# Performance work log

Hardware: AMD Instinct MI355X
Metric: run time of the kernel (lower is better)

The kernel has to match this reference:

```python
import jax, jax.numpy as jnp
import numpy as np

NUM_STEPS = 5
N_NODES = 50000
N_EDGES = 1250000
D_FEAT = 64


def setup_inputs() -> dict:
    key = jax.random.key(0)
    k1, k2, k3, k4 = jax.random.split(key, 4)
    x = jax.random.normal(k1, (N_NODES, D_FEAT), dtype=jnp.float32)
    edge_vals = jax.random.uniform(k2, (N_EDGES,), dtype=jnp.float32)
    edge_rows = jax.random.randint(k3, (N_EDGES,), 0, N_NODES, dtype=jnp.int32)
    edge_cols = jax.random.randint(k4, (N_EDGES,), 0, N_NODES, dtype=jnp.int32)
    return {"x": x, "edge_vals": edge_vals, "edge_rows": edge_rows, "edge_cols": edge_cols}


def reference(x, edge_vals, edge_rows, edge_cols):
    # Repeated SpMM: x <- A @ x, with A given in COO form (rows, cols, vals).
    # torch.sparse.mm(A, x)[i] = sum_{e: rows[e]==i} vals[e] * x[cols[e]]
    n = x.shape[0]

    def spmm(h):
        msgs = edge_vals[:, None] * h[edge_cols]          # [E, D] gather + scale
        return jax.ops.segment_sum(msgs, edge_rows, num_segments=n)  # [N, D] scatter-add

    for _ in range(NUM_STEPS):
        x = spmm(x)
    return x
```

## Files before the change

kernel.cpp:

```cpp
#include <hip/hip_runtime.h>
#include <hip/hip_fp16.h>
#include <stdint.h>

#define D_FEAT 64
#define CH 4096
#define BKT_BITS 8

__global__ __launch_bounds__(256) void bhist_kernel(const int* __restrict__ rows,
                                                    int* __restrict__ block_hist,
                                                    int n_edges, int nb) {
    __shared__ int cnt[256];
    cnt[threadIdx.x] = 0;
    __syncthreads();
    int beg = blockIdx.x * CH;
    int end = min(beg + CH, n_edges);
    for (int i = beg + threadIdx.x; i < end; i += 256)
        atomicAdd(&cnt[rows[i] >> BKT_BITS], 1);
    __syncthreads();
    if (threadIdx.x < nb)
        block_hist[blockIdx.x * nb + threadIdx.x] = cnt[threadIdx.x];
}

__global__ __launch_bounds__(256) void bscan1_kernel(int* __restrict__ block_hist,
                                                     int* __restrict__ btot,
                                                     int nchunks, int nb) {
    __shared__ int buf[256];
    int j = blockIdx.x;
    int t = threadIdx.x;
    int c0 = 2 * t, c1 = 2 * t + 1;
    int v0 = (c0 < nchunks) ? block_hist[(size_t)c0 * nb + j] : 0;
    int v1 = (c1 < nchunks) ? block_hist[(size_t)c1 * nb + j] : 0;
    int loc = v0 + v1;
    buf[t] = loc;
    __syncthreads();
    for (int off = 1; off < 256; off <<= 1) {
        int add = (t >= off) ? buf[t - off] : 0;
        __syncthreads();
        buf[t] += add;
        __syncthreads();
    }
    int excl = buf[t] - loc;
    if (c0 < nchunks) block_hist[(size_t)c0 * nb + j] = excl;
    if (c1 < nchunks) block_hist[(size_t)c1 * nb + j] = excl + v0;
    if (t == 255) btot[j] = buf[255];
}

__global__ __launch_bounds__(256) void bscan2_kernel(const int* __restrict__ btot,
                                                     int* __restrict__ bbase, int nb) {
    __shared__ int buf[256];
    int t = threadIdx.x;
    int v = (t < nb) ? btot[t] : 0;
    buf[t] = v;
    __syncthreads();
    for (int off = 1; off < 256; off <<= 1) {
        int add = (t >= off) ? buf[t - off] : 0;
        __syncthreads();
        buf[t] += add;
        __syncthreads();
    }
    if (t < nb) {
        bbase[t] = buf[t] - v;
        if (t == nb - 1) bbase[nb] = buf[t];
    }
}

__global__ __launch_bounds__(256) void bplace_kernel(const float* __restrict__ vals,
                                                     const int* __restrict__ rows,
                                                     const int* __restrict__ cols,
                                                     const int* __restrict__ block_hist,
                                                     const int* __restrict__ bbase,
                                                     uint2* __restrict__ mid,
                                                     int n_edges, int nb) {
    __shared__ int cnt[256];
    __shared__ int base[256];
    int t = threadIdx.x;
    cnt[t] = 0;
    if (t < nb) base[t] = bbase[t] + block_hist[(size_t)blockIdx.x * nb + t];
    __syncthreads();
    int beg = blockIdx.x * CH;
    int end = min(beg + CH, n_edges);
    for (int i = beg + t; i < end; i += 256) {
        int r = rows[i];
        int b = r >> BKT_BITS;
        int lrank = atomicAdd(&cnt[b], 1);
        __half hv = __float2half_rn(vals[i]);
        unsigned short vb = *reinterpret_cast<unsigned short*>(&hv);
        uint32_t packed = (uint32_t)(cols[i] & 0xFFFF) | ((uint32_t)vb << 16);
        mid[base[b] + lrank] = make_uint2(packed, (uint32_t)r);
    }
}

__global__ __launch_bounds__(256) void bsort_kernel(const uint2* __restrict__ mid,
                                                    const int* __restrict__ bbase,
                                                    uint32_t* __restrict__ edges,
                                                    int* __restrict__ offs,
                                                    int n_nodes, int nb) {
    __shared__ int cnt[256];
    __shared__ int start[256];
    __shared__ int buf[256];
    int j = blockIdx.x;
    int t = threadIdx.x;
    int lo = bbase[j];
    int hi = bbase[j + 1];
    cnt[t] = 0;
    __syncthreads();
    const uint32_t RMASK = (1u << BKT_BITS) - 1u;
    for (int i = lo + t; i < hi; i += 256)
        atomicAdd(&cnt[mid[i].y & RMASK], 1);
    __syncthreads();
    int v = cnt[t];
    buf[t] = v;
    __syncthreads();
    for (int off = 1; off < 256; off <<= 1) {
        int add = (t >= off) ? buf[t - off] : 0;
        __syncthreads();
        buf[t] += add;
        __syncthreads();
    }
    int st = buf[t] - v;
    start[t] = st;
    int rg = (j << BKT_BITS) + t;
    if (rg <= n_nodes) offs[rg] = lo + st;
    __syncthreads();
    cnt[t] = 0;
    __syncthreads();
    for (int i = lo + t; i < hi; i += 256) {
        uint2 e = mid[i];
        int r = (int)(e.y & RMASK);
        int rank = atomicAdd(&cnt[r], 1);
        edges[lo + start[r] + rank] = e.x;
    }
}


__device__ __forceinline__ float unpack_val(uint32_t u) {
    __half_raw hr;
    hr.x = (unsigned short)(u >> 16);
    return __half2float(__half(hr));
}

__device__ __forceinline__ float2 ld_bypass_f2(const float2* p) {
    unsigned long long v = __hip_atomic_load((const unsigned long long*)p,
                                             __ATOMIC_RELAXED, __HIP_MEMORY_SCOPE_AGENT);
    union { unsigned long long u; float2 f; } c;
    c.u = v;
    return c.f;
}
__device__ __forceinline__ __half2 ld_bypass_h2(const __half2* p) {
    uint32_t v = __hip_atomic_load((const uint32_t*)p,
                                   __ATOMIC_RELAXED, __HIP_MEMORY_SCOPE_AGENT);
    union { uint32_t u; __half2 h; } c;
    c.u = v;
    return c.h;
}

template <int K, bool IN_F32>
__device__ __forceinline__ void gfma2(const void* __restrict__ hv,
                                      const uint32_t* __restrict__ edges,
                                      int j, int gl, float2& acc) {
    uint32_t u[K];
#pragma unroll
    for (int k = 0; k < K; ++k) u[k] = edges[j + k];
    float2 hh[K];
#pragma unroll
    for (int k = 0; k < K; ++k) {
        size_t c = (size_t)(u[k] & 0xFFFF);
        if (IN_F32) hh[k] = ld_bypass_f2(((const float2*)hv) + c * 32 + gl);
        else        hh[k] = __half22float2(ld_bypass_h2(((const __half2*)hv) + c * 32 + gl));
    }
#pragma unroll
    for (int k = 0; k < K; ++k) {
        float v = unpack_val(u[k]);
        acc.x = fmaf(v, hh[k].x, acc.x);
        acc.y = fmaf(v, hh[k].y, acc.y);
    }
}

template <bool IN_F32, bool OUT_F32>
__global__ __launch_bounds__(256) void spmm2_kernel(const void* __restrict__ hv,
                                                    const uint32_t* __restrict__ edges,
                                                    const int* __restrict__ offs,
                                                    void* __restrict__ outv, int n_nodes) {
    int wave = (int)(((long long)blockIdx.x * blockDim.x + threadIdx.x) >> 6);
    int lane = threadIdx.x & 63;
    int g = lane >> 5;
    int gl = lane & 31;
    int row = wave * 2 + g;
    if (row >= n_nodes) return;
    int beg = offs[row];
    int end = offs[row + 1];
    float2 acc = make_float2(0.f, 0.f);
    int j = beg;
    for (; j + 8 <= end; j += 8) gfma2<8, IN_F32>(hv, edges, j, gl, acc);
    if (j + 4 <= end) { gfma2<4, IN_F32>(hv, edges, j, gl, acc); j += 4; }
    for (; j < end; ++j) {
        uint32_t u = edges[j];
        size_t c = (size_t)(u & 0xFFFF);
        float2 hh = IN_F32 ? ld_bypass_f2(((const float2*)hv) + c * 32 + gl)
                           : __half22float2(ld_bypass_h2(((const __half2*)hv) + c * 32 + gl));
        float v = unpack_val(u);
        acc.x = fmaf(v, hh.x, acc.x);
        acc.y = fmaf(v, hh.y, acc.y);
    }
    if (OUT_F32) {
        ((float2*)outv)[(size_t)row * 32 + gl] = acc;
    } else {
        ((__half2*)outv)[(size_t)row * 32 + gl] = __float22half2_rn(acc);
    }
}


__global__ void spmm_atomic_kernel(const float* __restrict__ h,
                                   const float* __restrict__ vals,
                                   const int* __restrict__ rows,
                                   const int* __restrict__ cols,
                                   float* __restrict__ out,
                                   int n_edges) {
    long long tid = (long long)blockIdx.x * blockDim.x + threadIdx.x;
    int e = (int)(tid >> 6);
    int d = (int)(tid & 63);
    if (e >= n_edges) return;
    float m = vals[e] * h[(size_t)cols[e] * D_FEAT + d];
    atomicAdd(&out[(size_t)rows[e] * D_FEAT + d], m);
}

extern "C" void kernel_launch(void* const* d_in, const int* in_sizes, int n_in,
                              void* d_out, int out_size, void* d_ws, size_t ws_size,
                              hipStream_t stream) {
    const float* x    = (const float*)d_in[0];
    const float* vals = (const float*)d_in[1];
    const int*   rows = (const int*)d_in[2];
    const int*   cols = (const int*)d_in[3];

    int n_nodes = in_sizes[0] / D_FEAT;
    int n_edges = in_sizes[1];

    float* out = (float*)d_out;

    size_t buf_bytes_f32 = (size_t)n_nodes * D_FEAT * sizeof(float);
    size_t buf_bytes_f16 = (size_t)n_nodes * D_FEAT * sizeof(__half);

    auto align_up = [](size_t v) { return (v + 255) & ~(size_t)255; };

    int nb = (n_nodes + 255) >> BKT_BITS;
    int nchunks = (n_edges + CH - 1) / CH;

    size_t pa_b   = align_up(buf_bytes_f16);
    size_t pb_b   = align_up(buf_bytes_f16);
    size_t mid_b  = align_up((size_t)n_edges * sizeof(uint2));
    size_t region1 = pa_b + pb_b;
    if (mid_b > region1) region1 = mid_b;
    size_t edges_b = align_up((size_t)n_edges * sizeof(uint32_t));
    size_t offs_b  = align_up((size_t)(n_nodes + 1) * sizeof(int));
    size_t bh_b    = align_up((size_t)nchunks * nb * sizeof(int));
    size_t bb_b    = align_up((size_t)(nb + 1) * sizeof(int));
    size_t bt_b    = align_up(256 * sizeof(int));
    size_t need = region1 + edges_b + offs_b + bh_b + bb_b + bt_b;

    if (ws_size < need || n_nodes > 65536 || nchunks > 512) {
        float* ws = (float*)d_ws;
        float* dsts[5] = {out, ws, out, ws, out};
        long long total_threads = (long long)n_edges * D_FEAT;
        int block = 256;
        int grid = (int)((total_threads + block - 1) / block);
        const float* src = x;
        for (int s = 0; s < 5; ++s) {
            hipMemsetAsync(dsts[s], 0, buf_bytes_f32, stream);
            spmm_atomic_kernel<<<grid, block, 0, stream>>>(src, vals, rows, cols,
                                                           dsts[s], n_edges);
            src = dsts[s];
        }
        return;
    }

    char* p = (char*)d_ws;
    char* r1 = p;                        p += region1;
    uint32_t* edges      = (uint32_t*)p; p += edges_b;
    int*      offs       = (int*)p;      p += offs_b;
    int*      block_hist = (int*)p;      p += bh_b;
    int*      bbase      = (int*)p;      p += bb_b;
    int*      btot       = (int*)p;      p += bt_b;

    __half2* pA = (__half2*)r1;
    __half2* pB = (__half2*)(r1 + pa_b);
    uint2*   mid = (uint2*)r1;

    bhist_kernel<<<nchunks, 256, 0, stream>>>(rows, block_hist, n_edges, nb);
    bscan1_kernel<<<nb, 256, 0, stream>>>(block_hist, btot, nchunks, nb);
    bscan2_kernel<<<1, 256, 0, stream>>>(btot, bbase, nb);
    bplace_kernel<<<nchunks, 256, 0, stream>>>(vals, rows, cols, block_hist, bbase,
                                               mid, n_edges, nb);
    bsort_kernel<<<nb, 256, 0, stream>>>(mid, bbase, edges, offs, n_nodes, nb);

    {
        int rows_per_block = 8;
        int grid = (n_nodes + rows_per_block - 1) / rows_per_block;
        spmm2_kernel<true,  false><<<grid, 256, 0, stream>>>(x,  edges, offs, pA, n_nodes);
        spmm2_kernel<false, false><<<grid, 256, 0, stream>>>(pA, edges, offs, pB, n_nodes);
        spmm2_kernel<false, false><<<grid, 256, 0, stream>>>(pB, edges, offs, pA, n_nodes);
        spmm2_kernel<false, false><<<grid, 256, 0, stream>>>(pA, edges, offs, pB, n_nodes);
        spmm2_kernel<false, true ><<<grid, 256, 0, stream>>>(pB, edges, offs, out, n_nodes);
    }
}
```

Measured before the change: 245.8 us.

## Assign one wave per row with 8-edge parallel gathers and shuffle reduction

Rewrites the SpMM kernel so each 64-lane wave handles one row. Eight subgroups of 8 lanes each gather a different edge's feature row with 16-byte vector loads, then the partial sums are combined by xor-shuffles. Ordinary cached loads replace the atomic bypass loads. The change aims for wider memory transactions and more gathers in flight per wave, at the cost of shuffle-reduction overhead and redundant lanes at the store.

```diff
diff --git a/kernel.cpp b/kernel.cpp
--- a/kernel.cpp
+++ b/kernel.cpp
@@ -139,73 +139,102 @@
     return __half2float(__half(hr));
 }
 
-__device__ __forceinline__ float2 ld_bypass_f2(const float2* p) {
-    unsigned long long v = __hip_atomic_load((const unsigned long long*)p,
-                                             __ATOMIC_RELAXED, __HIP_MEMORY_SCOPE_AGENT);
-    union { unsigned long long u; float2 f; } c;
-    c.u = v;
-    return c.f;
-}
-__device__ __forceinline__ __half2 ld_bypass_h2(const __half2* p) {
-    uint32_t v = __hip_atomic_load((const uint32_t*)p,
-                                   __ATOMIC_RELAXED, __HIP_MEMORY_SCOPE_AGENT);
-    union { uint32_t u; __half2 h; } c;
-    c.u = v;
-    return c.h;
-}
-
-template <int K, bool IN_F32>
-__device__ __forceinline__ void gfma2(const void* __restrict__ hv,
-                                      const uint32_t* __restrict__ edges,
-                                      int j, int gl, float2& acc) {
-    uint32_t u[K];
-#pragma unroll
-    for (int k = 0; k < K; ++k) u[k] = edges[j + k];
-    float2 hh[K];
-#pragma unroll
-    for (int k = 0; k < K; ++k) {
-        size_t c = (size_t)(u[k] & 0xFFFF);
-        if (IN_F32) hh[k] = ld_bypass_f2(((const float2*)hv) + c * 32 + gl);
-        else        hh[k] = __half22float2(ld_bypass_h2(((const __half2*)hv) + c * 32 + gl));
-    }
-#pragma unroll
-    for (int k = 0; k < K; ++k) {
-        float v = unpack_val(u[k]);
-        acc.x = fmaf(v, hh[k].x, acc.x);
-        acc.y = fmaf(v, hh[k].y, acc.y);
-    }
+__device__ __forceinline__ float2 h2f(uint32_t w) {
+    __half2 h = *reinterpret_cast<__half2*>(&w);
+    return __half22float2(h);
+}
+
+__device__ __forceinline__ uint32_t f2h2(float a, float b) {
+    __half2 h = __float22half2_rn(make_float2(a, b));
+    return *reinterpret_cast<uint32_t*>(&h);
+}
+
+__device__ __forceinline__ void fma8_h(const uint4& q, float v, float* acc) {
+    float2 f;
+    f = h2f(q.x); acc[0] = fmaf(v, f.x, acc[0]); acc[1] = fmaf(v, f.y, acc[1]);
+    f = h2f(q.y); acc[2] = fmaf(v, f.x, acc[2]); acc[3] = fmaf(v, f.y, acc[3]);
+    f = h2f(q.z); acc[4] = fmaf(v, f.x, acc[4]); acc[5] = fmaf(v, f.y, acc[5]);
+    f = h2f(q.w); acc[6] = fmaf(v, f.x, acc[6]); acc[7] = fmaf(v, f.y, acc[7]);
+}
+
+__device__ __forceinline__ void fma8_f(const float4& q0, const float4& q1, float v, float* acc) {
+    acc[0] = fmaf(v, q0.x, acc[0]); acc[1] = fmaf(v, q0.y, acc[1]);
+    acc[2] = fmaf(v, q0.z, acc[2]); acc[3] = fmaf(v, q0.w, acc[3]);
+    acc[4] = fmaf(v, q1.x, acc[4]); acc[5] = fmaf(v, q1.y, acc[5]);
+    acc[6] = fmaf(v, q1.z, acc[6]); acc[7] = fmaf(v, q1.w, acc[7]);
 }
 
 template <bool IN_F32, bool OUT_F32>
-__global__ __launch_bounds__(256) void spmm2_kernel(const void* __restrict__ hv,
+__global__ __launch_bounds__(256) void spmm8_kernel(const void* __restrict__ hv,
                                                     const uint32_t* __restrict__ edges,
                                                     const int* __restrict__ offs,
                                                     void* __restrict__ outv, int n_nodes) {
-    int wave = (int)(((long long)blockIdx.x * blockDim.x + threadIdx.x) >> 6);
+    int row = (int)(((long long)blockIdx.x * blockDim.x + threadIdx.x) >> 6);
+    if (row >= n_nodes) return;
     int lane = threadIdx.x & 63;
-    int g = lane >> 5;
-    int gl = lane & 31;
-    int row = wave * 2 + g;
-    if (row >= n_nodes) return;
-    int beg = offs[row];
-    int end = offs[row + 1];
-    float2 acc = make_float2(0.f, 0.f);
-    int j = beg;
-    for (; j + 8 <= end; j += 8) gfma2<8, IN_F32>(hv, edges, j, gl, acc);
-    if (j + 4 <= end) { gfma2<4, IN_F32>(hv, edges, j, gl, acc); j += 4; }
-    for (; j < end; ++j) {
-        uint32_t u = edges[j];
-        size_t c = (size_t)(u & 0xFFFF);
-        float2 hh = IN_F32 ? ld_bypass_f2(((const float2*)hv) + c * 32 + gl)
-                           : __half22float2(ld_bypass_h2(((const __half2*)hv) + c * 32 + gl));
-        float v = unpack_val(u);
-        acc.x = fmaf(v, hh.x, acc.x);
-        acc.y = fmaf(v, hh.y, acc.y);
-    }
+    int sg = lane >> 3;
+    int fl = lane & 7;
+
+    int beg = offs[row], end = offs[row + 1];
+    float acc[8] = {0.f, 0.f, 0.f, 0.f, 0.f, 0.f, 0.f, 0.f};
+
+    int j0 = beg;
+    for (; j0 + 16 <= end; j0 += 16) {
+        uint32_t ua = edges[j0 + sg];
+        uint32_t ub = edges[j0 + 8 + sg];
+        if (IN_F32) {
+            const float4* hp = (const float4*)hv;
+            size_t ca = (size_t)(ua & 0xFFFF) * 16 + fl * 2;
+            size_t cb = (size_t)(ub & 0xFFFF) * 16 + fl * 2;
+            float4 qa0 = hp[ca], qa1 = hp[ca + 1];
+            float4 qb0 = hp[cb], qb1 = hp[cb + 1];
+            fma8_f(qa0, qa1, unpack_val(ua), acc);
+            fma8_f(qb0, qb1, unpack_val(ub), acc);
+        } else {
+            const uint4* hp = (const uint4*)hv;
+            uint4 qa = hp[(size_t)(ua & 0xFFFF) * 8 + fl];
+            uint4 qb = hp[(size_t)(ub & 0xFFFF) * 8 + fl];
+            fma8_h(qa, unpack_val(ua), acc);
+            fma8_h(qb, unpack_val(ub), acc);
+        }
+    }
+    for (; j0 < end; j0 += 8) {
+        int j = j0 + sg;
+        if (j < end) {
+            uint32_t u = edges[j];
+            float v = unpack_val(u);
+            if (IN_F32) {
+                const float4* hp = (const float4*)hv;
+                size_t c = (size_t)(u & 0xFFFF) * 16 + fl * 2;
+                float4 q0 = hp[c], q1 = hp[c + 1];
+                fma8_f(q0, q1, v, acc);
+            } else {
+                const uint4* hp = (const uint4*)hv;
+                uint4 q = hp[(size_t)(u & 0xFFFF) * 8 + fl];
+                fma8_h(q, v, acc);
+            }
+        }
+    }
+
+#pragma unroll
+    for (int m = 8; m <= 32; m <<= 1) {
+#pragma unroll
+        for (int i = 0; i < 8; ++i) acc[i] += __shfl_xor(acc[i], m, 64);
+    }
+
     if (OUT_F32) {
-        ((float2*)outv)[(size_t)row * 32 + gl] = acc;
+        float4* op = (float4*)outv + (size_t)row * 16 + fl * 2;
+        if (sg == 0) op[0] = make_float4(acc[0], acc[1], acc[2], acc[3]);
+        else if (sg == 1) op[1] = make_float4(acc[4], acc[5], acc[6], acc[7]);
     } else {
-        ((__half2*)outv)[(size_t)row * 32 + gl] = __float22half2_rn(acc);
+        if (sg == 0) {
+            uint4 o;
+            o.x = f2h2(acc[0], acc[1]);
+            o.y = f2h2(acc[2], acc[3]);
+            o.z = f2h2(acc[4], acc[5]);
+            o.w = f2h2(acc[6], acc[7]);
+            ((uint4*)outv)[(size_t)row * 8 + fl] = o;
+        }
     }
 }
 
@@ -281,9 +310,9 @@
     int*      bbase      = (int*)p;      p += bb_b;
     int*      btot       = (int*)p;      p += bt_b;
 
-    __half2* pA = (__half2*)r1;
-    __half2* pB = (__half2*)(r1 + pa_b);
-    uint2*   mid = (uint2*)r1;
+    __half* pA = (__half*)r1;
+    __half* pB = (__half*)(r1 + pa_b);
+    uint2*  mid = (uint2*)r1;
 
     bhist_kernel<<<nchunks, 256, 0, stream>>>(rows, block_hist, n_edges, nb);
     bscan1_kernel<<<nb, 256, 0, stream>>>(block_hist, btot, nchunks, nb);
@@ -293,12 +322,12 @@
     bsort_kernel<<<nb, 256, 0, stream>>>(mid, bbase, edges, offs, n_nodes, nb);
 
     {
-        int rows_per_block = 8;
+        int rows_per_block = 4;
         int grid = (n_nodes + rows_per_block - 1) / rows_per_block;
-        spmm2_kernel<true,  false><<<grid, 256, 0, stream>>>(x,  edges, offs, pA, n_nodes);
-        spmm2_kernel<false, false><<<grid, 256, 0, stream>>>(pA, edges, offs, pB, n_nodes);
-        spmm2_kernel<false, false><<<grid, 256, 0, stream>>>(pB, edges, offs, pA, n_nodes);
-        spmm2_kernel<false, false><<<grid, 256, 0, stream>>>(pA, edges, offs, pB, n_nodes);
-        spmm2_kernel<false, true ><<<grid, 256, 0, stream>>>(pB, edges, offs, out, n_nodes);
-    }
-}
+        spmm8_kernel<true,  false><<<grid, 256, 0, stream>>>(x,  edges, offs, pA, n_nodes);
+        spmm8_kernel<false, false><<<grid, 256, 0, stream>>>(pA, edges, offs, pB, n_nodes);
+        spmm8_kernel<false, false><<<grid, 256, 0, stream>>>(pB, edges, offs, pA, n_nodes);
+        spmm8_kernel<false, false><<<grid, 256, 0, stream>>>(pA, edges, offs, pB, n_nodes);
+        spmm8_kernel<false, true ><<<grid, 256, 0, stream>>>(pB, edges, offs, out, n_nodes);
+    }
+}
```

After: 252.6 us. +2.8%, slower.

## Pre-cast input to fp16 and use cached gathers with nontemporal edge loads

Applied to the files above, without the earlier changes.

Adds a small kernel that converts the fp32 input to fp16 once, so all five SpMM steps gather half-precision rows and the first step no longer reads fp32. The agent-scope atomic 'bypass' loads used for feature gathers are replaced with ordinary cached loads, so gathered rows can hit in cache. Edge-list reads become nontemporal so they do not evict feature data. The main loop is also unrolled to 16 edges per iteration for more loads in flight. The costs are an extra kernel launch, a full pass over x, and rounding x to fp16 before the first step.

```diff
diff --git a/kernel.cpp b/kernel.cpp
--- a/kernel.cpp
+++ b/kernel.cpp
@@ -132,6 +132,13 @@
     }
 }
 
+__global__ __launch_bounds__(256) void xcast_kernel(const float2* __restrict__ x,
+                                                    __half2* __restrict__ dst, int total_h2) {
+    int t = blockIdx.x * 256 + threadIdx.x;
+    if (t >= total_h2) return;
+    dst[t] = __float22half2_rn(x[t]);
+}
+
 
 __device__ __forceinline__ float unpack_val(uint32_t u) {
     __half_raw hr;
@@ -139,35 +146,17 @@
     return __half2float(__half(hr));
 }
 
-__device__ __forceinline__ float2 ld_bypass_f2(const float2* p) {
-    unsigned long long v = __hip_atomic_load((const unsigned long long*)p,
-                                             __ATOMIC_RELAXED, __HIP_MEMORY_SCOPE_AGENT);
-    union { unsigned long long u; float2 f; } c;
-    c.u = v;
-    return c.f;
-}
-__device__ __forceinline__ __half2 ld_bypass_h2(const __half2* p) {
-    uint32_t v = __hip_atomic_load((const uint32_t*)p,
-                                   __ATOMIC_RELAXED, __HIP_MEMORY_SCOPE_AGENT);
-    union { uint32_t u; __half2 h; } c;
-    c.u = v;
-    return c.h;
-}
-
-template <int K, bool IN_F32>
-__device__ __forceinline__ void gfma2(const void* __restrict__ hv,
-                                      const uint32_t* __restrict__ edges,
-                                      int j, int gl, float2& acc) {
+template <int K>
+__device__ __forceinline__ void gfma2h(const __half2* __restrict__ hv,
+                                       const uint32_t* __restrict__ edges,
+                                       int j, int gl, float2& acc) {
     uint32_t u[K];
 #pragma unroll
-    for (int k = 0; k < K; ++k) u[k] = edges[j + k];
+    for (int k = 0; k < K; ++k) u[k] = __builtin_nontemporal_load(&edges[j + k]);
     float2 hh[K];
 #pragma unroll
-    for (int k = 0; k < K; ++k) {
-        size_t c = (size_t)(u[k] & 0xFFFF);
-        if (IN_F32) hh[k] = ld_bypass_f2(((const float2*)hv) + c * 32 + gl);
-        else        hh[k] = __half22float2(ld_bypass_h2(((const __half2*)hv) + c * 32 + gl));
-    }
+    for (int k = 0; k < K; ++k)
+        hh[k] = __half22float2(hv[(size_t)(u[k] & 0xFFFF) * 32 + gl]);
 #pragma unroll
     for (int k = 0; k < K; ++k) {
         float v = unpack_val(u[k]);
@@ -176,11 +165,11 @@
     }
 }
 
-template <bool IN_F32, bool OUT_F32>
-__global__ __launch_bounds__(256) void spmm2_kernel(const void* __restrict__ hv,
-                                                    const uint32_t* __restrict__ edges,
-                                                    const int* __restrict__ offs,
-                                                    void* __restrict__ outv, int n_nodes) {
+template <bool OUT_F32>
+__global__ __launch_bounds__(256) void spmm_h_kernel(const __half2* __restrict__ hv,
+                                                     const uint32_t* __restrict__ edges,
+                                                     const int* __restrict__ offs,
+                                                     void* __restrict__ outv, int n_nodes) {
     int wave = (int)(((long long)blockIdx.x * blockDim.x + threadIdx.x) >> 6);
     int lane = threadIdx.x & 63;
     int g = lane >> 5;
@@ -191,13 +180,15 @@
     int end = offs[row + 1];
     float2 acc = make_float2(0.f, 0.f);
     int j = beg;
-    for (; j + 8 <= end; j += 8) gfma2<8, IN_F32>(hv, edges, j, gl, acc);
-    if (j + 4 <= end) { gfma2<4, IN_F32>(hv, edges, j, gl, acc); j += 4; }
+    for (; j + 16 <= end; j += 16) {
+        gfma2h<8>(hv, edges, j, gl, acc);
+        gfma2h<8>(hv, edges, j + 8, gl, acc);
+    }
+    if (j + 8 <= end) { gfma2h<8>(hv, edges, j, gl, acc); j += 8; }
+    if (j + 4 <= end) { gfma2h<4>(hv, edges, j, gl, acc); j += 4; }
     for (; j < end; ++j) {
-        uint32_t u = edges[j];
-        size_t c = (size_t)(u & 0xFFFF);
-        float2 hh = IN_F32 ? ld_bypass_f2(((const float2*)hv) + c * 32 + gl)
-                           : __half22float2(ld_bypass_h2(((const __half2*)hv) + c * 32 + gl));
+        uint32_t u = __builtin_nontemporal_load(&edges[j]);
+        float2 hh = __half22float2(hv[(size_t)(u & 0xFFFF) * 32 + gl]);
         float v = unpack_val(u);
         acc.x = fmaf(v, hh.x, acc.x);
         acc.y = fmaf(v, hh.y, acc.y);
@@ -293,12 +284,15 @@
     bsort_kernel<<<nb, 256, 0, stream>>>(mid, bbase, edges, offs, n_nodes, nb);
 
     {
+        int total_h2 = n_nodes * 32;
+        xcast_kernel<<<(total_h2 + 255) / 256, 256, 0, stream>>>((const float2*)x, pA, total_h2);
+
         int rows_per_block = 8;
         int grid = (n_nodes + rows_per_block - 1) / rows_per_block;
-        spmm2_kernel<true,  false><<<grid, 256, 0, stream>>>(x,  edges, offs, pA, n_nodes);
-        spmm2_kernel<false, false><<<grid, 256, 0, stream>>>(pA, edges, offs, pB, n_nodes);
-        spmm2_kernel<false, false><<<grid, 256, 0, stream>>>(pB, edges, offs, pA, n_nodes);
-        spmm2_kernel<false, false><<<grid, 256, 0, stream>>>(pA, edges, offs, pB, n_nodes);
-        spmm2_kernel<false, true ><<<grid, 256, 0, stream>>>(pB, edges, offs, out, n_nodes);
-    }
-}
+        spmm_h_kernel<false><<<grid, 256, 0, stream>>>(pA, edges, offs, pB, n_nodes);
+        spmm_h_kernel<false><<<grid, 256, 0, stream>>>(pB, edges, offs, pA, n_nodes);
+        spmm_h_kernel<false><<<grid, 256, 0, stream>>>(pA, edges, offs, pB, n_nodes);
+        spmm_h_kernel<false><<<grid, 256, 0, stream>>>(pB, edges, offs, pA, n_nodes);
+        spmm_h_kernel<true ><<<grid, 256, 0, stream>>>(pA, edges, offs, out, n_nodes);
+    }
+}
```

New measurement: 263.0 us. 1.07x slower.
